# Kernel optimization log

Hardware: AMD Instinct MI355X
Metric: run time of the kernel (lower is better)

The kernel has to match this reference:

```python
import jax, jax.numpy as jnp
import numpy as np

N = 50000          # num_nodes
E = 800000         # num_edges (avg degree 16)
HID = 128          # hidden_dim
NH = 8             # num_heads
HD = 16            # head_dim
FFN = 512          # ffn_dim
EPS = 1e-5


def setup_inputs() -> dict:
    key = jax.random.key(0)
    ks = jax.random.split(key, 12)
    s = 0.02
    d = {}
    d["x"] = jax.random.normal(ks[0], (N, HID), jnp.float32)
    d["edge_index"] = jax.random.randint(ks[1], (2, E), 0, N, dtype=jnp.int32)
    # projection weights stored as [in, out] (math identical to torch Linear)
    d["Wq"] = jax.random.normal(ks[2], (HID, NH * HD), jnp.float32) * s
    d["bq"] = jnp.zeros((NH * HD,), jnp.float32)
    d["Wk"] = jax.random.normal(ks[3], (HID, NH * HD), jnp.float32) * s
    d["bk"] = jnp.zeros((NH * HD,), jnp.float32)
    d["Wv"] = jax.random.normal(ks[4], (HID, NH * HD), jnp.float32) * s
    d["bv"] = jnp.zeros((NH * HD,), jnp.float32)
    d["Wo"] = jax.random.normal(ks[5], (NH * HD, HID), jnp.float32) * s
    d["bo"] = jnp.zeros((HID,), jnp.float32)
    d["g1"] = jnp.ones((HID,), jnp.float32)
    d["b1"] = jnp.zeros((HID,), jnp.float32)
    d["g2"] = jnp.ones((HID,), jnp.float32)
    d["b2"] = jnp.zeros((HID,), jnp.float32)
    d["W1"] = jax.random.normal(ks[6], (HID, FFN), jnp.float32) * s
    d["bf1"] = jnp.zeros((FFN,), jnp.float32)
    d["W2"] = jax.random.normal(ks[7], (FFN, HID), jnp.float32) * s
    d["bf2"] = jnp.zeros((HID,), jnp.float32)
    return d


def _layer_norm(x, g, b):
    m = jnp.mean(x, axis=-1, keepdims=True)
    v = jnp.mean((x - m) ** 2, axis=-1, keepdims=True)
    return (x - m) * jax.lax.rsqrt(v + EPS) * g + b


def _gnn_layer(x, edge_index, Wq, bq, Wk, bk, Wv, bv, Wo, bo,
               g1, b1, g2, b2, W1, bf1, W2, bf2):
    n = x.shape[0]
    residual = x
    h = _layer_norm(x, g1, b1)

    q = (h @ Wq + bq).reshape(n, NH, HD)
    k = (h @ Wk + bk).reshape(n, NH, HD)
    v = (h @ Wv + bv).reshape(n, NH, HD)

    src, dst = edge_index[0], edge_index[1]
    # original code skips nodes with no in-neighbors (output stays zero)
    deg = jax.ops.segment_sum(jnp.ones(src.shape, x.dtype), dst, num_segments=n)
    # self-loop appended for every attended node
    loops = jnp.arange(n, dtype=src.dtype)
    s_all = jnp.concatenate([src, loops])
    d_all = jnp.concatenate([dst, loops])

    # edge-parallel scaled dot-product scores: [E+N, NH]
    e = jnp.sum(q[d_all] * k[s_all], axis=-1) / np.sqrt(HD).astype(np.float32)
    m = jax.lax.stop_gradient(jax.ops.segment_max(e, d_all, num_segments=n))
    p = jnp.exp(e - m[d_all])
    z = jax.ops.segment_sum(p, d_all, num_segments=n)
    alpha = p / z[d_all]                                   # segment softmax
    agg = jax.ops.segment_sum(alpha[:, :, None] * v[s_all], d_all,
                              num_segments=n)              # [n, NH, HD]
    agg = jnp.where(deg[:, None, None] > 0, agg, jnp.zeros_like(agg))

    att = agg.reshape(n, NH * HD) @ Wo + bo
    x = residual + att                                     # dropout=0 (eval)

    residual = x
    h = _layer_norm(x, g2, b2)
    ffn = jax.nn.gelu(h @ W1 + bf1, approximate=False) @ W2 + bf2
    return residual + ffn


def reference(x, edge_index, Wq, bq, Wk, bk, Wv, bv, Wo, bo,
              g1, b1, g2, b2, W1, bf1, W2, bf2):
    return _gnn_layer(x, edge_index, Wq, bq, Wk, bk, Wv, bv, Wo, bo,
                      g1, b1, g2, b2, W1, bf1, W2, bf2)
```

## Files before the change

kernel.cpp:

```cpp
#include <hip/hip_runtime.h>
#include <hip/hip_bf16.h>

typedef __hip_bfloat16 bf16;
typedef __attribute__((ext_vector_type(8))) short s16x8;
typedef __attribute__((ext_vector_type(4))) float f32x4;

__device__ __forceinline__ float2 bfpair(unsigned u) {
    float2 r;
    r.x = __uint_as_float(u << 16);
    r.y = __uint_as_float(u & 0xffff0000u);
    return r;
}

__device__ __forceinline__ unsigned short f2bf_bits(float f) {
    unsigned u = __float_as_uint(f);
    return (unsigned short)((u + 0x7fffu + ((u >> 16) & 1u)) >> 16);
}

typedef const __attribute__((address_space(1))) unsigned GU;
typedef __attribute__((address_space(3))) unsigned LU;
__device__ __forceinline__ void gload_lds16(const void* g, void* l) {
    __builtin_amdgcn_global_load_lds((GU*)g, (LU*)l, 16, 0, 0);
}

__global__ __launch_bounds__(256) void setup_k(const float* __restrict__ Wq,
                                               const float* __restrict__ Wk,
                                               const float* __restrict__ Wv,
                                               const float* __restrict__ Wo,
                                               const float* __restrict__ W1,
                                               const float* __restrict__ W2,
                                               const float* __restrict__ bq,
                                               const float* __restrict__ bk,
                                               const float* __restrict__ bv,
                                               unsigned short* __restrict__ qkvH,
                                               unsigned short* __restrict__ qkvL,
                                               unsigned short* __restrict__ woH,
                                               unsigned short* __restrict__ woL,
                                               unsigned short* __restrict__ w1H,
                                               unsigned short* __restrict__ w1L,
                                               unsigned short* __restrict__ w2H,
                                               unsigned short* __restrict__ w2L,
                                               float* __restrict__ bqkv,
                                               int* __restrict__ deg,
                                               const unsigned* __restrict__ eisrc,
                                               int* __restrict__ ei32,
                                               int N, int twoE, int nzero) {
    int b = blockIdx.x;
    int tid = threadIdx.x;
    if (b < 770) {
        int idx = b * 256 + tid;
        if (idx >= 196608) {
            int i = idx - 196608;
            if (i < 384) bqkv[i] = (i < 128) ? bq[i] : (i < 256) ? bk[i - 128] : bv[i - 256];
            return;
        }
        float w; unsigned short *H, *L; int oi;
        if (idx < 49152) {
            int n = idx >> 7, kx = idx & 127;
            const float* W = (n < 128) ? Wq : (n < 256) ? Wk : Wv;
            w = W[kx * 128 + (n & 127)];
            H = qkvH; L = qkvL; oi = idx;
        } else if (idx < 65536) {
            int li = idx - 49152; int n = li >> 7, kx = li & 127;
            w = Wo[kx * 128 + n]; H = woH; L = woL; oi = li;
        } else if (idx < 131072) {
            int li = idx - 65536; int n = li >> 7, kx = li & 127;
            w = W1[(size_t)kx * 512 + n]; H = w1H; L = w1L; oi = li;
        } else {
            int li = idx - 131072; int n = li >> 9, kx = li & 511;
            w = W2[(size_t)kx * 128 + n]; H = w2H; L = w2L; oi = li;
        }
        unsigned short hbits = f2bf_bits(w);
        float hf = __uint_as_float((unsigned)hbits << 16);
        H[oi] = hbits;
        L[oi] = f2bf_bits(w - hf);
        return;
    }
    if (b < 770 + nzero) {
        int i = (b - 770) * 256 + tid;
        if (i < N) deg[i] = 0;
        return;
    }
    __shared__ int s_nz;
    if (tid == 0) s_nz = 0;
    __syncthreads();
    if (eisrc[2 * tid + 1] != 0u) atomicAdd(&s_nz, 1);
    __syncthreads();
    bool is64 = (s_nz == 0);
    long long i = (long long)(b - 770 - nzero) * 256 + tid;
    long long st = (long long)2000 * 256;
    if (is64) { for (; i < twoE; i += st) ei32[i] = (int)eisrc[2 * i]; }
    else      { for (; i < twoE; i += st) ei32[i] = (int)eisrc[i]; }
}

__global__ __launch_bounds__(256) void count_deg_k(const int* __restrict__ ei,
                                                   int* __restrict__ deg, int E) {
    int e = blockIdx.x * 256 + threadIdx.x;
    if (e < E) atomicAdd(&deg[ei[E + e]], 1);
}

#define SCAN_BLK 1024
__global__ __launch_bounds__(256) void scan1_k(const int* __restrict__ deg,
                                               int* __restrict__ off,
                                               int* __restrict__ bsum, int n) {
    __shared__ int s[256];
    int base = blockIdx.x * SCAN_BLK;
    int t = threadIdx.x;
    int v[4]; int sum = 0;
    #pragma unroll
    for (int j = 0; j < 4; j++) {
        int idx = base + t * 4 + j;
        v[j] = (idx < n) ? deg[idx] : 0;
        sum += v[j];
    }
    s[t] = sum; __syncthreads();
    for (int o = 1; o < 256; o <<= 1) {
        int add = (t >= o) ? s[t - o] : 0;
        __syncthreads();
        s[t] += add;
        __syncthreads();
    }
    int run = (t > 0) ? s[t - 1] : 0;
    if (t == 255) bsum[blockIdx.x] = s[255];
    #pragma unroll
    for (int j = 0; j < 4; j++) {
        int idx = base + t * 4 + j;
        if (idx < n) off[idx] = run;
        run += v[j];
    }
}

__global__ __launch_bounds__(256) void scan3_k(int* __restrict__ off,
                                               int* __restrict__ cursor,
                                               const int* __restrict__ bsum,
                                               int n, int nb) {
    __shared__ int sb[64];
    int t = threadIdx.x;
    if (t < 64) {
        int own = (t < nb) ? bsum[t] : 0;
        int v = own;
        #pragma unroll
        for (int o = 1; o < 64; o <<= 1) {
            int u = __shfl_up(v, o);
            if ((t & 63) >= o) v += u;
        }
        sb[t] = v - own;
    }
    __syncthreads();
    int i = blockIdx.x * 256 + t;
    if (i < n) {
        int o = off[i] + sb[i / SCAN_BLK];
        off[i] = o;
        cursor[i] = o;
    }
}

__global__ __launch_bounds__(256) void scatter_k(const int* __restrict__ ei,
                                                 int* __restrict__ cursor,
                                                 int* __restrict__ csr, int E) {
    int e = blockIdx.x * 256 + threadIdx.x;
    if (e >= E) return;
    int s = ei[e], d = ei[E + e];
    int pos = atomicAdd(&cursor[d], 1);
    csr[pos] = s;
}

__global__ __launch_bounds__(256) void ln_bf16_k(const float* __restrict__ x,
                                                 const float* __restrict__ g,
                                                 const float* __restrict__ b,
                                                 bf16* __restrict__ out, int M) {
    int row = blockIdx.x * 4 + (threadIdx.x >> 6);
    if (row >= M) return;
    int lane = threadIdx.x & 63;
    float2 f = ((const float2*)x)[(size_t)row * 64 + lane];
    float s = f.x + f.y;
    #pragma unroll
    for (int off = 32; off > 0; off >>= 1) s += __shfl_xor(s, off);
    float mean = s * (1.0f / 128.0f);
    float d0 = f.x - mean, d1 = f.y - mean;
    float vs = d0 * d0 + d1 * d1;
    #pragma unroll
    for (int off = 32; off > 0; off >>= 1) vs += __shfl_xor(vs, off);
    float rstd = rsqrtf(vs * (1.0f / 128.0f) + 1e-5f);
    float2 gg = ((const float2*)g)[lane];
    float2 bb = ((const float2*)b)[lane];
    float o0 = d0 * rstd * gg.x + bb.x;
    float o1 = d1 * rstd * gg.y + bb.y;
    unsigned pk = ((unsigned)f2bf_bits(o1) << 16) | (unsigned)f2bf_bits(o0);
    ((unsigned*)out)[(size_t)row * 64 + lane] = pk;
}

template <int EPI, bool OUTBF, int K, int BM, bool LNF>
__global__ __launch_bounds__(256) void mgemm_k(const bf16* __restrict__ A,
                                               const bf16* __restrict__ Bh,
                                               const bf16* __restrict__ Bl,
                                               const float* __restrict__ bias,
                                               const float* __restrict__ res,
                                               void* __restrict__ outp,
                                               const float* __restrict__ lg,
                                               const float* __restrict__ lb,
                                               bf16* __restrict__ hbout,
                                               long long sub_off, int M,
                                               int ldo, int sub_shift) {
    constexpr int MF = BM / 32;
    constexpr int NK = K / 32;
    constexpr int STEP = BM * 64 + 2 * 8192;
    __shared__ __align__(16) char smem[2 * STEP];

    const int lane = threadIdx.x & 63;
    const int wid  = threadIdx.x >> 6;
    const int wr = wid >> 1, wc = wid & 1;
    const int lrow = lane & 15, lk = lane >> 4;
    const int m0 = blockIdx.y * BM;
    const int mw0 = wr * (BM / 2);
    const int n0 = blockIdx.x * 128 + wc * 64;
    const int srow = lane >> 2;
    const int schunk = (lane & 3) ^ (srow & 3);

    const char* Ab  = (const char*)A  + (size_t)m0 * (K * 2);
    const char* Bhb = (const char*)Bh + (size_t)(blockIdx.x * 128) * (K * 2);
    const char* Blb = (const char*)Bl + (size_t)(blockIdx.x * 128) * (K * 2);

    f32x4 acc[MF][4];
    #pragma unroll
    for (int mf = 0; mf < MF; mf++)
        #pragma unroll
        for (int nf = 0; nf < 4; nf++) {
            f32x4 z = {0.f, 0.f, 0.f, 0.f};
            acc[mf][nf] = z;
        }

    auto stage = [&](int kt, int bufb) {
        const int kb = kt * 64;
        char* sb = &smem[bufb];
        #pragma unroll
        for (int it = 0; it < BM / 64; it++) {
            int rg = wid * (BM / 4) + it * 16;
            gload_lds16(Ab + (size_t)(rg + srow) * (K * 2) + kb + schunk * 16,
                        sb + rg * 64);
        }
        #pragma unroll
        for (int it = 0; it < 2; it++) {
            int rg = wid * 32 + it * 16;
            gload_lds16(Bhb + (size_t)(rg + srow) * (K * 2) + kb + schunk * 16,
                        sb + BM * 64 + rg * 64);
            gload_lds16(Blb + (size_t)(rg + srow) * (K * 2) + kb + schunk * 16,
                        sb + BM * 64 + 8192 + rg * 64);
        }
    };

    auto compute = [&](int bufb) {
        const char* sb = &smem[bufb];
        s16x8 a[MF], bh[4], bl[4];
        #pragma unroll
        for (int mf = 0; mf < MF; mf++) {
            int ra = mw0 + mf * 16 + lrow;
            a[mf] = *(const s16x8*)(sb + ra * 64 + ((lk ^ (ra & 3)) * 16));
        }
        #pragma unroll
        for (int nf = 0; nf < 4; nf++) {
            int rb = wc * 64 + nf * 16 + lrow;
            int co = (lk ^ (rb & 3)) * 16;
            bh[nf] = *(const s16x8*)(sb + BM * 64 + rb * 64 + co);
            bl[nf] = *(const s16x8*)(sb + BM * 64 + 8192 + rb * 64 + co);
        }
        #pragma unroll
        for (int mf = 0; mf < MF; mf++)
            #pragma unroll
            for (int nf = 0; nf < 4; nf++)
                acc[mf][nf] = __builtin_amdgcn_mfma_f32_16x16x32_bf16(a[mf], bh[nf], acc[mf][nf], 0, 0, 0);
        #pragma unroll
        for (int mf = 0; mf < MF; mf++)
            #pragma unroll
            for (int nf = 0; nf < 4; nf++)
                acc[mf][nf] = __builtin_amdgcn_mfma_f32_16x16x32_bf16(a[mf], bl[nf], acc[mf][nf], 0, 0, 0);
    };

    stage(0, 0);
    for (int kt = 0; kt < NK; kt++) {
        __syncthreads();
        if (kt + 1 < NK) stage(kt + 1, ((kt + 1) & 1) * STEP);
        compute((kt & 1) * STEP);
    }

    if (!LNF) {
        const int nmask = (1 << sub_shift) - 1;
        #pragma unroll
        for (int mf = 0; mf < MF; mf++) {
            #pragma unroll
            for (int nf = 0; nf < 4; nf++) {
                int n = n0 + nf * 16 + lrow;
                float bsv = bias[n];
                #pragma unroll
                for (int r = 0; r < 4; r++) {
                    int m = m0 + mw0 + mf * 16 + lk * 4 + r;
                    if (m >= M) continue;
                    float val = acc[mf][nf][r] + bsv;
                    if (EPI == 1) val = 0.5f * val * (1.0f + erff(val * 0.70710678118f));
                    if (EPI == 2) val += res[(size_t)m * ldo + n];
                    long long oidx = (long long)m * ldo + (n & nmask) + (long long)(n >> sub_shift) * sub_off;
                    if (OUTBF) ((unsigned short*)outp)[oidx] = f2bf_bits(val);
                    else       ((float*)outp)[oidx] = val;
                }
            }
        }
    } else {
        float vals[MF][4][4];
        float s1[MF][4], s2[MF][4];
        #pragma unroll
        for (int mf = 0; mf < MF; mf++)
            #pragma unroll
            for (int r = 0; r < 4; r++) { s1[mf][r] = 0.f; s2[mf][r] = 0.f; }
        #pragma unroll
        for (int mf = 0; mf < MF; mf++) {
            #pragma unroll
            for (int r = 0; r < 4; r++) {
                int m = m0 + mw0 + mf * 16 + lk * 4 + r;
                #pragma unroll
                for (int nf = 0; nf < 4; nf++) {
                    int n = n0 + nf * 16 + lrow;
                    float val = acc[mf][nf][r] + bias[n];
                    val += (m < M) ? res[(size_t)m * 128 + n] : 0.f;
                    vals[mf][nf][r] = val;
                    s1[mf][r] += val;
                    s2[mf][r] += val * val;
                }
                #pragma unroll
                for (int o = 1; o < 16; o <<= 1) {
                    s1[mf][r] += __shfl_xor(s1[mf][r], o);
                    s2[mf][r] += __shfl_xor(s2[mf][r], o);
                }
            }
        }
        float2* lns = (float2*)smem;
        __syncthreads();
        if (lrow == 0) {
            #pragma unroll
            for (int mf = 0; mf < MF; mf++)
                #pragma unroll
                for (int r = 0; r < 4; r++) {
                    int rl = mw0 + mf * 16 + lk * 4 + r;
                    float2 p; p.x = s1[mf][r]; p.y = s2[mf][r];
                    lns[rl * 2 + wc] = p;
                }
        }
        __syncthreads();
        #pragma unroll
        for (int mf = 0; mf < MF; mf++) {
            #pragma unroll
            for (int r = 0; r < 4; r++) {
                int rl = mw0 + mf * 16 + lk * 4 + r;
                int m = m0 + rl;
                float2 pa = lns[rl * 2 + 0], pb = lns[rl * 2 + 1];
                float mean = (pa.x + pb.x) * (1.0f / 128.0f);
                float var  = (pa.y + pb.y) * (1.0f / 128.0f) - mean * mean;
                float rstd = rsqrtf(var + 1e-5f);
                if (m >= M) continue;
                #pragma unroll
                for (int nf = 0; nf < 4; nf++) {
                    int n = n0 + nf * 16 + lrow;
                    float val = vals[mf][nf][r];
                    ((float*)outp)[(size_t)m * 128 + n] = val;
                    float o = (val - mean) * rstd * lg[n] + lb[n];
                    ((unsigned short*)hbout)[(size_t)m * 128 + n] = f2bf_bits(o);
                }
            }
        }
    }
}

__global__ __launch_bounds__(256) void node_agg_k(const bf16* __restrict__ q,
                                                  const bf16* __restrict__ k,
                                                  const bf16* __restrict__ v,
                                                  const int* __restrict__ off,
                                                  const int* __restrict__ deg,
                                                  const int* __restrict__ csr,
                                                  bf16* __restrict__ agg, int NN) {
    int node = blockIdx.x * 4 + (threadIdx.x >> 6);
    if (node >= NN) return;
    int lane = threadIdx.x & 63;
    float2 qf = bfpair(((const unsigned*)(q + (size_t)node * 128))[lane]);
    int start = off[node];
    int cnt = deg[node];
    float acc0 = 0.f, acc1 = 0.f, zsum = 0.f;
    if (cnt < 64) {
        int T = cnt + 1;
        int s_vec = (lane < cnt) ? csr[start + lane] : node;
        for (int e0 = 0; e0 < T; e0 += 8) {
            unsigned ku[8], vu[8];
            #pragma unroll
            for (int j = 0; j < 8; j++) {
                if (e0 + j < T) {
                    int s = __shfl(s_vec, e0 + j);
                    ku[j] = ((const unsigned*)(k + (size_t)s * 128))[lane];
                    vu[j] = ((const unsigned*)(v + (size_t)s * 128))[lane];
                }
            }
            #pragma unroll
            for (int j = 0; j < 8; j++) {
                if (e0 + j < T) {
                    float2 kf = bfpair(ku[j]);
                    float dot = qf.x * kf.x + qf.y * kf.y;
                    dot += __shfl_xor(dot, 1);
                    dot += __shfl_xor(dot, 2);
                    dot += __shfl_xor(dot, 4);
                    float p = __expf(dot * 0.25f);
                    zsum += p;
                    float2 vf = bfpair(vu[j]);
                    acc0 += p * vf.x;
                    acc1 += p * vf.y;
                }
            }
        }
    } else {
        for (int e = 0; e <= cnt; e++) {
            int s = (e < cnt) ? csr[start + e] : node;
            float2 kf = bfpair(((const unsigned*)(k + (size_t)s * 128))[lane]);
            float dot = qf.x * kf.x + qf.y * kf.y;
            dot += __shfl_xor(dot, 1);
            dot += __shfl_xor(dot, 2);
            dot += __shfl_xor(dot, 4);
            float p = __expf(dot * 0.25f);
            zsum += p;
            float2 vf = bfpair(((const unsigned*)(v + (size_t)s * 128))[lane]);
            acc0 += p * vf.x;
            acc1 += p * vf.y;
        }
    }
    float2 o;
    if (cnt == 0) { o.x = 0.f; o.y = 0.f; }
    else { float inv = 1.0f / zsum; o.x = acc0 * inv; o.y = acc1 * inv; }
    unsigned pk = ((unsigned)f2bf_bits(o.y) << 16) | (unsigned)f2bf_bits(o.x);
    ((unsigned*)agg)[(size_t)node * 64 + lane] = pk;
}

extern "C" void kernel_launch(void* const* d_in, const int* in_sizes, int n_in,
                              void* d_out, int out_size, void* d_ws, size_t ws_size,
                              hipStream_t stream) {
    const float* x  = (const float*)d_in[0];
    const void*  eiRaw = d_in[1];
    const float* Wq = (const float*)d_in[2];
    const float* bq = (const float*)d_in[3];
    const float* Wk = (const float*)d_in[4];
    const float* bk = (const float*)d_in[5];
    const float* Wv = (const float*)d_in[6];
    const float* bv = (const float*)d_in[7];
    const float* Wo = (const float*)d_in[8];
    const float* bo = (const float*)d_in[9];
    const float* g1 = (const float*)d_in[10];
    const float* b1 = (const float*)d_in[11];
    const float* g2 = (const float*)d_in[12];
    const float* b2 = (const float*)d_in[13];
    const float* W1 = (const float*)d_in[14];
    const float* bf1 = (const float*)d_in[15];
    const float* W2 = (const float*)d_in[16];
    const float* bf2 = (const float*)d_in[17];
    float* out = (float*)d_out;

    const int N = in_sizes[0] / 128;
    const int E = in_sizes[1] / 2;
    const int gy = (N + 127) / 128;
    const int gy64 = (N + 63) / 64;
    const int Mp = gy * 128;

    char* w = (char*)d_ws;
    size_t off_b = 0;
    auto alloc = [&](size_t bytes) -> void* {
        void* ptr = w + off_b;
        off_b = (off_b + bytes + 255) & ~(size_t)255;
        return ptr;
    };
    int*   deg    = (int*)alloc((size_t)N * 4);
    int*   offA   = (int*)alloc((size_t)N * 4);
    int*   cursor = (int*)alloc((size_t)N * 4);
    int*   bsum   = (int*)alloc(64 * 4);
    int*   ei32   = (int*)alloc((size_t)E * 2 * 4);
    int*   csr    = (int*)alloc((size_t)E * 4);
    bf16*  hb     = (bf16*)alloc((size_t)Mp * 128 * 2);
    bf16*  qkvb   = (bf16*)alloc((size_t)N * 3 * 128 * 2);
    bf16*  aggb   = (bf16*)alloc((size_t)Mp * 128 * 2);
    bf16*  t      = (bf16*)alloc((size_t)Mp * 512 * 2);
    unsigned short* qkvH = (unsigned short*)alloc(49152 * 2);
    unsigned short* qkvL = (unsigned short*)alloc(49152 * 2);
    unsigned short* woH  = (unsigned short*)alloc(16384 * 2);
    unsigned short* woL  = (unsigned short*)alloc(16384 * 2);
    unsigned short* w1H  = (unsigned short*)alloc(65536 * 2);
    unsigned short* w1L  = (unsigned short*)alloc(65536 * 2);
    unsigned short* w2H  = (unsigned short*)alloc(65536 * 2);
    unsigned short* w2L  = (unsigned short*)alloc(65536 * 2);
    float* bqkv = (float*)alloc(384 * 4);
    (void)ws_size; (void)n_in; (void)out_size;

    int nb = (N + SCAN_BLK - 1) / SCAN_BLK;
    int nzero = (N + 255) / 256;

    setup_k<<<770 + nzero + 2000, 256, 0, stream>>>(
        Wq, Wk, Wv, Wo, W1, W2, bq, bk, bv,
        qkvH, qkvL, woH, woL, w1H, w1L, w2H, w2L, bqkv,
        deg, (const unsigned*)eiRaw, ei32, N, E * 2, nzero);
    count_deg_k<<<(E + 255) / 256, 256, 0, stream>>>(ei32, deg, E);
    scan1_k<<<nb, 256, 0, stream>>>(deg, offA, bsum, N);
    scan3_k<<<(N + 255) / 256, 256, 0, stream>>>(offA, cursor, bsum, N, nb);
    scatter_k<<<(E + 255) / 256, 256, 0, stream>>>(ei32, cursor, csr, E);

    bf16* qb = qkvb;
    bf16* kb = qkvb + (size_t)N * 128;
    bf16* vb = qkvb + (size_t)N * 256;

    ln_bf16_k<<<(N + 3) / 4, 256, 0, stream>>>(x, g1, b1, hb, N);
    mgemm_k<0, true, 128, 128, false><<<dim3(3, gy), 256, 0, stream>>>(
        hb, (const bf16*)qkvH, (const bf16*)qkvL, bqkv, nullptr, qkvb,
        nullptr, nullptr, nullptr, (long long)N * 128, N, 128, 7);
    node_agg_k<<<(N + 3) / 4, 256, 0, stream>>>(qb, kb, vb, offA, deg, csr, aggb, N);
    mgemm_k<2, false, 128, 64, true><<<dim3(1, gy64), 256, 0, stream>>>(
        aggb, (const bf16*)woH, (const bf16*)woL, bo, x, out,
        g2, b2, hb, 0, N, 128, 15);
    mgemm_k<1, true, 128, 128, false><<<dim3(4, gy), 256, 0, stream>>>(
        hb, (const bf16*)w1H, (const bf16*)w1L, bf1, nullptr, t,
        nullptr, nullptr, nullptr, 0, N, 512, 15);
    mgemm_k<2, false, 512, 64, false><<<dim3(1, gy64), 256, 0, stream>>>(
        t, (const bf16*)w2H, (const bf16*)w2L, bf2, out, out,
        nullptr, nullptr, nullptr, 0, N, 128, 15);
}
```

Before: 394.8 us.

## Interleave K/V rows, prescale Q, fold LayerNorm into setup, drop edge-index copy

New measurement: 440.2 us. 1.11x slower.

```diff
diff --git a/kernel.cpp b/kernel.cpp
--- a/kernel.cpp
+++ b/kernel.cpp
@@ -22,6 +22,8 @@
 __device__ __forceinline__ void gload_lds16(const void* g, void* l) {
     __builtin_amdgcn_global_load_lds((GU*)g, (LU*)l, 16, 0, 0);
 }
+
+#define QSCALE 0.36067376022f
 
 __global__ __launch_bounds__(256) void setup_k(const float* __restrict__ Wq,
                                                const float* __restrict__ Wk,
@@ -42,9 +44,11 @@
                                                unsigned short* __restrict__ w2L,
                                                float* __restrict__ bqkv,
                                                int* __restrict__ deg,
-                                               const unsigned* __restrict__ eisrc,
-                                               int* __restrict__ ei32,
-                                               int N, int twoE, int nzero) {
+                                               const float* __restrict__ x,
+                                               const float* __restrict__ g1,
+                                               const float* __restrict__ b1,
+                                               bf16* __restrict__ hb,
+                                               int N, int nzero) {
     int b = blockIdx.x;
     int tid = threadIdx.x;
     if (b < 770) {
@@ -81,22 +85,40 @@
         if (i < N) deg[i] = 0;
         return;
     }
+    int row = (b - 770 - nzero) * 4 + (tid >> 6);
+    if (row >= N) return;
+    int lane = tid & 63;
+    float2 f = ((const float2*)x)[(size_t)row * 64 + lane];
+    float s = f.x + f.y;
+    #pragma unroll
+    for (int off = 32; off > 0; off >>= 1) s += __shfl_xor(s, off);
+    float mean = s * (1.0f / 128.0f);
+    float d0 = f.x - mean, d1 = f.y - mean;
+    float vs = d0 * d0 + d1 * d1;
+    #pragma unroll
+    for (int off = 32; off > 0; off >>= 1) vs += __shfl_xor(vs, off);
+    float rstd = rsqrtf(vs * (1.0f / 128.0f) + 1e-5f);
+    float2 gg = ((const float2*)g1)[lane];
+    float2 bb = ((const float2*)b1)[lane];
+    float o0 = d0 * rstd * gg.x + bb.x;
+    float o1 = d1 * rstd * gg.y + bb.y;
+    unsigned pk = ((unsigned)f2bf_bits(o1) << 16) | (unsigned)f2bf_bits(o0);
+    ((unsigned*)hb)[(size_t)row * 64 + lane] = pk;
+}
+
+__global__ __launch_bounds__(256) void count_deg_k(const unsigned* __restrict__ ei,
+                                                   int* __restrict__ deg, int E) {
     __shared__ int s_nz;
-    if (tid == 0) s_nz = 0;
+    if (threadIdx.x == 0) s_nz = 0;
     __syncthreads();
-    if (eisrc[2 * tid + 1] != 0u) atomicAdd(&s_nz, 1);
+    if (ei[2 * threadIdx.x + 1] != 0u) atomicAdd(&s_nz, 1);
     __syncthreads();
     bool is64 = (s_nz == 0);
-    long long i = (long long)(b - 770 - nzero) * 256 + tid;
-    long long st = (long long)2000 * 256;
-    if (is64) { for (; i < twoE; i += st) ei32[i] = (int)eisrc[2 * i]; }
-    else      { for (; i < twoE; i += st) ei32[i] = (int)eisrc[i]; }
-}
-
-__global__ __launch_bounds__(256) void count_deg_k(const int* __restrict__ ei,
-                                                   int* __restrict__ deg, int E) {
     int e = blockIdx.x * 256 + threadIdx.x;
-    if (e < E) atomicAdd(&deg[ei[E + e]], 1);
+    if (e < E) {
+        int d = is64 ? (int)ei[2 * ((size_t)E + e)] : (int)ei[(size_t)E + e];
+        atomicAdd(&deg[d], 1);
+    }
 }
 
 #define SCAN_BLK 1024
@@ -155,42 +177,25 @@
     }
 }
 
-__global__ __launch_bounds__(256) void scatter_k(const int* __restrict__ ei,
+__global__ __launch_bounds__(256) void scatter_k(const unsigned* __restrict__ ei,
                                                  int* __restrict__ cursor,
                                                  int* __restrict__ csr, int E) {
+    __shared__ int s_nz;
+    if (threadIdx.x == 0) s_nz = 0;
+    __syncthreads();
+    if (ei[2 * threadIdx.x + 1] != 0u) atomicAdd(&s_nz, 1);
+    __syncthreads();
+    bool is64 = (s_nz == 0);
     int e = blockIdx.x * 256 + threadIdx.x;
     if (e >= E) return;
-    int s = ei[e], d = ei[E + e];
+    int s, d;
+    if (is64) { s = (int)ei[2 * (size_t)e]; d = (int)ei[2 * ((size_t)E + e)]; }
+    else      { s = (int)ei[e];             d = (int)ei[(size_t)E + e]; }
     int pos = atomicAdd(&cursor[d], 1);
     csr[pos] = s;
 }
 
-__global__ __launch_bounds__(256) void ln_bf16_k(const float* __restrict__ x,
-                                                 const float* __restrict__ g,
-                                                 const float* __restrict__ b,
-                                                 bf16* __restrict__ out, int M) {
-    int row = blockIdx.x * 4 + (threadIdx.x >> 6);
-    if (row >= M) return;
-    int lane = threadIdx.x & 63;
-    float2 f = ((const float2*)x)[(size_t)row * 64 + lane];
-    float s = f.x + f.y;
-    #pragma unroll
-    for (int off = 32; off > 0; off >>= 1) s += __shfl_xor(s, off);
-    float mean = s * (1.0f / 128.0f);
-    float d0 = f.x - mean, d1 = f.y - mean;
-    float vs = d0 * d0 + d1 * d1;
-    #pragma unroll
-    for (int off = 32; off > 0; off >>= 1) vs += __shfl_xor(vs, off);
-    float rstd = rsqrtf(vs * (1.0f / 128.0f) + 1e-5f);
-    float2 gg = ((const float2*)g)[lane];
-    float2 bb = ((const float2*)b)[lane];
-    float o0 = d0 * rstd * gg.x + bb.x;
-    float o1 = d1 * rstd * gg.y + bb.y;
-    unsigned pk = ((unsigned)f2bf_bits(o1) << 16) | (unsigned)f2bf_bits(o0);
-    ((unsigned*)out)[(size_t)row * 64 + lane] = pk;
-}
-
-template <int EPI, bool OUTBF, int K, int BM, bool LNF>
+template <int EPI, bool OUTBF, int K, int BM, bool LNF, int ROUTE>
 __global__ __launch_bounds__(256) void mgemm_k(const bf16* __restrict__ A,
                                                const bf16* __restrict__ Bh,
                                                const bf16* __restrict__ Bl,
@@ -199,9 +204,8 @@
                                                void* __restrict__ outp,
                                                const float* __restrict__ lg,
                                                const float* __restrict__ lb,
-                                               bf16* __restrict__ hbout,
-                                               long long sub_off, int M,
-                                               int ldo, int sub_shift) {
+                                               bf16* __restrict__ kvout,
+                                               int M, int ldo) {
     constexpr int MF = BM / 32;
     constexpr int NK = K / 32;
     constexpr int STEP = BM * 64 + 2 * 8192;
@@ -284,7 +288,6 @@
     }
 
     if (!LNF) {
-        const int nmask = (1 << sub_shift) - 1;
         #pragma unroll
         for (int mf = 0; mf < MF; mf++) {
             #pragma unroll
@@ -298,9 +301,16 @@
                     float val = acc[mf][nf][r] + bsv;
                     if (EPI == 1) val = 0.5f * val * (1.0f + erff(val * 0.70710678118f));
                     if (EPI == 2) val += res[(size_t)m * ldo + n];
-                    long long oidx = (long long)m * ldo + (n & nmask) + (long long)(n >> sub_shift) * sub_off;
-                    if (OUTBF) ((unsigned short*)outp)[oidx] = f2bf_bits(val);
-                    else       ((float*)outp)[oidx] = val;
+                    if (ROUTE == 1) {
+                        if (n < 128)
+                            ((unsigned short*)outp)[(size_t)m * 128 + n] = f2bf_bits(val * QSCALE);
+                        else
+                            ((unsigned short*)kvout)[(size_t)m * 256 + (n - 128)] = f2bf_bits(val);
+                    } else {
+                        size_t oidx = (size_t)m * ldo + n;
+                        if (OUTBF) ((unsigned short*)outp)[oidx] = f2bf_bits(val);
+                        else       ((float*)outp)[oidx] = val;
+                    }
                 }
             }
         }
@@ -362,7 +372,7 @@
                     float val = vals[mf][nf][r];
                     ((float*)outp)[(size_t)m * 128 + n] = val;
                     float o = (val - mean) * rstd * lg[n] + lb[n];
-                    ((unsigned short*)hbout)[(size_t)m * 128 + n] = f2bf_bits(o);
+                    ((unsigned short*)kvout)[(size_t)m * 128 + n] = f2bf_bits(o);
                 }
             }
         }
@@ -370,8 +380,7 @@
 }
 
 __global__ __launch_bounds__(256) void node_agg_k(const bf16* __restrict__ q,
-                                                  const bf16* __restrict__ k,
-                                                  const bf16* __restrict__ v,
+                                                  const bf16* __restrict__ kv,
                                                   const int* __restrict__ off,
                                                   const int* __restrict__ deg,
                                                   const int* __restrict__ csr,
@@ -379,59 +388,59 @@
     int node = blockIdx.x * 4 + (threadIdx.x >> 6);
     if (node >= NN) return;
     int lane = threadIdx.x & 63;
-    float2 qf = bfpair(((const unsigned*)(q + (size_t)node * 128))[lane]);
+    float4 q4 = make_float4(0.f, 0.f, 0.f, 0.f);
+    if (lane < 32) {
+        uint2 qu = ((const uint2*)(q + (size_t)node * 128))[lane];
+        float2 a = bfpair(qu.x), b = bfpair(qu.y);
+        q4.x = a.x; q4.y = a.y; q4.z = b.x; q4.w = b.y;
+    }
     int start = off[node];
     int cnt = deg[node];
-    float acc0 = 0.f, acc1 = 0.f, zsum = 0.f;
+    const char* kvb = (const char*)kv;
+    const unsigned laneoff = lane * 8u;
+    float a0 = 0.f, a1 = 0.f, a2 = 0.f, a3 = 0.f, zs = 0.f;
+
+    auto body = [&](uint2 u) {
+        float2 xa = bfpair(u.x), xb = bfpair(u.y);
+        float r = q4.x * xa.x + q4.y * xa.y + q4.z * xb.x + q4.w * xb.y;
+        r += __shfl_xor(r, 1);
+        r += __shfl_xor(r, 2);
+        float p;
+        asm("v_exp_f32 %0, %1" : "=v"(p) : "v"(r));
+        p = __shfl(p, lane & 31);
+        zs += p;
+        a0 += p * xa.x; a1 += p * xa.y; a2 += p * xb.x; a3 += p * xb.y;
+    };
+
     if (cnt < 64) {
         int T = cnt + 1;
         int s_vec = (lane < cnt) ? csr[start + lane] : node;
         for (int e0 = 0; e0 < T; e0 += 8) {
-            unsigned ku[8], vu[8];
-            #pragma unroll
-            for (int j = 0; j < 8; j++) {
+            uint2 u[8];
+            #pragma unroll
+            for (int j = 0; j < 8; j++)
                 if (e0 + j < T) {
                     int s = __shfl(s_vec, e0 + j);
-                    ku[j] = ((const unsigned*)(k + (size_t)s * 128))[lane];
-                    vu[j] = ((const unsigned*)(v + (size_t)s * 128))[lane];
+                    u[j] = *(const uint2*)(kvb + (size_t)s * 512 + laneoff);
                 }
-            }
-            #pragma unroll
-            for (int j = 0; j < 8; j++) {
-                if (e0 + j < T) {
-                    float2 kf = bfpair(ku[j]);
-                    float dot = qf.x * kf.x + qf.y * kf.y;
-                    dot += __shfl_xor(dot, 1);
-                    dot += __shfl_xor(dot, 2);
-                    dot += __shfl_xor(dot, 4);
-                    float p = __expf(dot * 0.25f);
-                    zsum += p;
-                    float2 vf = bfpair(vu[j]);
-                    acc0 += p * vf.x;
-                    acc1 += p * vf.y;
-                }
-            }
+            #pragma unroll
+            for (int j = 0; j < 8; j++)
+                if (e0 + j < T) body(u[j]);
         }
     } else {
         for (int e = 0; e <= cnt; e++) {
             int s = (e < cnt) ? csr[start + e] : node;
-            float2 kf = bfpair(((const unsigned*)(k + (size_t)s * 128))[lane]);
-            float dot = qf.x * kf.x + qf.y * kf.y;
-            dot += __shfl_xor(dot, 1);
-            dot += __shfl_xor(dot, 2);
-            dot += __shfl_xor(dot, 4);
-            float p = __expf(dot * 0.25f);
-            zsum += p;
-            float2 vf = bfpair(((const unsigned*)(v + (size_t)s * 128))[lane]);
-            acc0 += p * vf.x;
-            acc1 += p * vf.y;
-        }
-    }
-    float2 o;
-    if (cnt == 0) { o.x = 0.f; o.y = 0.f; }
-    else { float inv = 1.0f / zsum; o.x = acc0 * inv; o.y = acc1 * inv; }
-    unsigned pk = ((unsigned)f2bf_bits(o.y) << 16) | (unsigned)f2bf_bits(o.x);
-    ((unsigned*)agg)[(size_t)node * 64 + lane] = pk;
+            uint2 u = *(const uint2*)(kvb + (size_t)s * 512 + laneoff);
+            body(u);
+        }
+    }
+    if (lane >= 32) {
+        float inv = (cnt == 0) ? 0.f : 1.0f / zs;
+        unsigned lo = ((unsigned)f2bf_bits(a1 * inv) << 16) | f2bf_bits(a0 * inv);
+        unsigned hi = ((unsigned)f2bf_bits(a3 * inv) << 16) | f2bf_bits(a2 * inv);
+        uint2 o; o.x = lo; o.y = hi;
+        ((uint2*)((char*)agg + (size_t)node * 256))[lane - 32] = o;
+    }
 }
 
 extern "C" void kernel_launch(void* const* d_in, const int* in_sizes, int n_in,
@@ -474,10 +483,10 @@
     int*   offA   = (int*)alloc((size_t)N * 4);
     int*   cursor = (int*)alloc((size_t)N * 4);
     int*   bsum   = (int*)alloc(64 * 4);
-    int*   ei32   = (int*)alloc((size_t)E * 2 * 4);
     int*   csr    = (int*)alloc((size_t)E * 4);
     bf16*  hb     = (bf16*)alloc((size_t)Mp * 128 * 2);
-    bf16*  qkvb   = (bf16*)alloc((size_t)N * 3 * 128 * 2);
+    bf16*  qb     = (bf16*)alloc((size_t)N * 128 * 2);
+    bf16*  kvb    = (bf16*)alloc((size_t)N * 256 * 2);
     bf16*  aggb   = (bf16*)alloc((size_t)Mp * 128 * 2);
     bf16*  t      = (bf16*)alloc((size_t)Mp * 512 * 2);
     unsigned short* qkvH = (unsigned short*)alloc(49152 * 2);
@@ -493,32 +502,28 @@
 
     int nb = (N + SCAN_BLK - 1) / SCAN_BLK;
     int nzero = (N + 255) / 256;
-
-    setup_k<<<770 + nzero + 2000, 256, 0, stream>>>(
+    int lnb = (N + 3) / 4;
+
+    setup_k<<<770 + nzero + lnb, 256, 0, stream>>>(
         Wq, Wk, Wv, Wo, W1, W2, bq, bk, bv,
         qkvH, qkvL, woH, woL, w1H, w1L, w2H, w2L, bqkv,
-        deg, (const unsigned*)eiRaw, ei32, N, E * 2, nzero);
-    count_deg_k<<<(E + 255) / 256, 256, 0, stream>>>(ei32, deg, E);
+        deg, x, g1, b1, hb, N, nzero);
+    count_deg_k<<<(E + 255) / 256, 256, 0, stream>>>((const unsigned*)eiRaw, deg, E);
     scan1_k<<<nb, 256, 0, stream>>>(deg, offA, bsum, N);
     scan3_k<<<(N + 255) / 256, 256, 0, stream>>>(offA, cursor, bsum, N, nb);
-    scatter_k<<<(E + 255) / 256, 256, 0, stream>>>(ei32, cursor, csr, E);
-
-    bf16* qb = qkvb;
-    bf16* kb = qkvb + (size_t)N * 128;
-    bf16* vb = qkvb + (size_t)N * 256;
-
-    ln_bf16_k<<<(N + 3) / 4, 256, 0, stream>>>(x, g1, b1, hb, N);
-    mgemm_k<0, true, 128, 128, false><<<dim3(3, gy), 256, 0, stream>>>(
-        hb, (const bf16*)qkvH, (const bf16*)qkvL, bqkv, nullptr, qkvb,
-        nullptr, nullptr, nullptr, (long long)N * 128, N, 128, 7);
-    node_agg_k<<<(N + 3) / 4, 256, 0, stream>>>(qb, kb, vb, offA, deg, csr, aggb, N);
-    mgemm_k<2, false, 128, 64, true><<<dim3(1, gy64), 256, 0, stream>>>(
+    scatter_k<<<(E + 255) / 256, 256, 0, stream>>>((const unsigned*)eiRaw, cursor, csr, E);
+
+    mgemm_k<0, true, 128, 128, false, 1><<<dim3(3, gy), 256, 0, stream>>>(
+        hb, (const bf16*)qkvH, (const bf16*)qkvL, bqkv, nullptr, qb,
+        nullptr, nullptr, kvb, N, 128);
+    node_agg_k<<<(N + 3) / 4, 256, 0, stream>>>(qb, kvb, offA, deg, csr, aggb, N);
+    mgemm_k<2, false, 128, 64, true, 0><<<dim3(1, gy64), 256, 0, stream>>>(
         aggb, (const bf16*)woH, (const bf16*)woL, bo, x, out,
-        g2, b2, hb, 0, N, 128, 15);
-    mgemm_k<1, true, 128, 128, false><<<dim3(4, gy), 256, 0, stream>>>(
+        g2, b2, hb, N, 128);
+    mgemm_k<1, true, 128, 128, false, 0><<<dim3(4, gy), 256, 0, stream>>>(
         hb, (const bf16*)w1H, (const bf16*)w1L, bf1, nullptr, t,
-        nullptr, nullptr, nullptr, 0, N, 512, 15);
-    mgemm_k<2, false, 512, 64, false><<<dim3(1, gy64), 256, 0, stream>>>(
+        nullptr, nullptr, nullptr, N, 512);
+    mgemm_k<2, false, 512, 64, false, 0><<<dim3(1, gy64), 256, 0, stream>>>(
         t, (const bf16*)w2H, (const bf16*)w2L, bf2, out, out,
-        nullptr, nullptr, nullptr, 0, N, 128, 15);
-}
+        nullptr, nullptr, nullptr, N, 128);
+}
```
